# Kernel tuning notes

Measured on AMD Instinct MI355X. Metric: run time of the kernel, lower is better.

Reference implementation:

```python
import jax, jax.numpy as jnp
import numpy as np

B, D, K, E = 256, 256, 1024, 16  # batch, dim_codes, book_size, embedding_dim
DECAY = 0.999
GAIN = 1.0 - DECAY
EPS = 1e-6


def setup_inputs() -> dict:
    key = jax.random.key(0)
    k1, k2 = jax.random.split(key)
    return {
        "cw_q": jax.random.normal(k1, (B, D * E), dtype=jnp.float32),
        "codebook": jax.random.normal(k2, (D, K, E), dtype=jnp.float32),
        "ema_counts": jnp.ones((D, K), dtype=jnp.float32),
    }


def reference(cw_q, codebook, ema_counts):
    batch = cw_q.shape[0]
    x = cw_q.reshape(batch, D, E)  # [B, D, E]

    x2 = jnp.sum(x * x, axis=-1)                       # [B, D]
    c2 = jnp.sum(codebook * codebook, axis=-1)         # [D, K]
    xc = jnp.einsum('bde,dke->bdk', x, codebook)       # [B, D, K]
    dist = x2[:, :, None] + c2[None, :, :] - 2.0 * xc

    idx = jnp.argmin(dist, axis=-1)                    # [B, D] int32

    # gather nearest code vector per (batch, dim_code)
    cw_embed = codebook[jnp.arange(D)[None, :], idx]   # [B, D, E]
    cw_embed = cw_embed.reshape(batch, D * E)

    one_hot_idx = jax.nn.one_hot(idx, K, dtype=cw_q.dtype)  # [B, D, K]

    # EMA update (training path): scatter-sum of assigned vectors per code
    update = jnp.einsum('bdk,bde->dke', one_hot_idx, x)      # [D, K, E]
    new_codebook = codebook * DECAY + GAIN * update / (ema_counts[:, :, None] + EPS)
    new_ema_counts = DECAY * ema_counts + GAIN * jnp.sum(one_hot_idx, axis=0)

    return cw_embed, one_hot_idx, new_codebook, new_ema_counts
```

## Files before the change

kernel.cpp:

```cpp
#include <hip/hip_runtime.h>
#include <float.h>

#define BB 256
#define DD 256
#define KK 1024
#define EE 16
#define DECAY 0.999f
#define GAIN  0.001f
#define EPS   1e-6f

#define OH_OFF   ((size_t)BB * DD * EE)
#define CB_OFF   (OH_OFF + (size_t)BB * DD * KK)
#define EMA_OFF  (CB_OFF + (size_t)DD * KK * EE)

typedef float f32x4 __attribute__((ext_vector_type(4)));

__device__ __forceinline__ float dot16(const float4& a0, const float4& a1,
                                       const float4& a2, const float4& a3,
                                       const float4& b0, const float4& b1,
                                       const float4& b2, const float4& b3) {
  float s = a0.x * b0.x;
  s = fmaf(a0.y, b0.y, s); s = fmaf(a0.z, b0.z, s); s = fmaf(a0.w, b0.w, s);
  s = fmaf(a1.x, b1.x, s); s = fmaf(a1.y, b1.y, s); s = fmaf(a1.z, b1.z, s); s = fmaf(a1.w, b1.w, s);
  s = fmaf(a2.x, b2.x, s); s = fmaf(a2.y, b2.y, s); s = fmaf(a2.z, b2.z, s); s = fmaf(a2.w, b2.w, s);
  s = fmaf(a3.x, b3.x, s); s = fmaf(a3.y, b3.y, s); s = fmaf(a3.z, b3.z, s); s = fmaf(a3.w, b3.w, s);
  return s;
}

__device__ __forceinline__ unsigned long long packkey(float dist, int k) {
  unsigned u = __float_as_uint(dist);
  unsigned m = ((int)u < 0) ? 0xFFFFFFFFu : 0x80000000u;
  return ((unsigned long long)(u ^ m) << 32) | (unsigned long long)(unsigned)k;
}

__device__ __forceinline__ void ntst4(float4* p, float4 v) {
  f32x4 t = { v.x, v.y, v.z, v.w };
  __builtin_nontemporal_store(t, (f32x4*)p);
}

__global__ __launch_bounds__(1024) void vqvae_main(
    const float* __restrict__ cw_q,
    const float* __restrict__ codebook,
    const float* __restrict__ ema,
    float* __restrict__ out)
{
  __shared__ float4 cb4s[KK * EE / 4];
  __shared__ float4 upd4s[KK * EE / 4];
  __shared__ float  c2s[KK];
  __shared__ float  esh[KK];
  __shared__ float  cnts[KK];
  __shared__ unsigned long long amin[BB];
  __shared__ int    ish[BB];

  const int t = threadIdx.x;
  const int d = blockIdx.x;
  const int w = t >> 6;
  const int l = t & 63;
  const float4 z4 = make_float4(0.f, 0.f, 0.f, 0.f);

  cnts[t] = 0.f;
  if (t < BB) amin[t] = ~0ULL;
  esh[t] = ema[(size_t)d * KK + t];
  #pragma unroll
  for (int i = 0; i < 4; ++i) upd4s[i * 1024 + t] = z4;

  const float4* src4 = (const float4*)codebook + (size_t)d * (KK * EE / 4);
  #pragma unroll
  for (int i = 0; i < 4; ++i) {
    int i4 = i * 1024 + t;
    float4 v = src4[i4];
    cb4s[i4] = v;
    float sq = v.x * v.x;
    sq = fmaf(v.y, v.y, sq);
    sq = fmaf(v.z, v.z, sq);
    sq = fmaf(v.w, v.w, sq);
    sq += __shfl_xor(sq, 1);
    sq += __shfl_xor(sq, 2);
    if ((t & 3) == 0) c2s[i4 >> 2] = sq;
  }

  float4 xv[4][4];
  float  x2[4];
  #pragma unroll
  for (int j = 0; j < 4; ++j) {
    const int b = l + 64 * j;
    const float4* xr = (const float4*)cw_q + (size_t)b * (DD * EE / 4) + d * 4;
    xv[j][0] = xr[0]; xv[j][1] = xr[1]; xv[j][2] = xr[2]; xv[j][3] = xr[3];
  }
  #pragma unroll
  for (int j = 0; j < 4; ++j)
    x2[j] = dot16(xv[j][0], xv[j][1], xv[j][2], xv[j][3],
                  xv[j][0], xv[j][1], xv[j][2], xv[j][3]);

  __syncthreads();

  float best[4] = {FLT_MAX, FLT_MAX, FLT_MAX, FLT_MAX};
  int   bi[4]   = {0, 0, 0, 0};
  const int kbase = w << 6;

  #pragma unroll 2
  for (int s = 0; s < 64; ++s) {
    const int k = kbase + s;
    const float4* p = cb4s + (k << 2);
    float4 c0 = p[0], c1 = p[1], c2v = p[2], c3 = p[3];
    const float c2k = c2s[k];
    #pragma unroll
    for (int j = 0; j < 4; ++j) {
      float dj = dot16(c0, c1, c2v, c3, xv[j][0], xv[j][1], xv[j][2], xv[j][3]);
      float dist = fmaf(-2.f, dj, x2[j] + c2k);
      if (dist < best[j]) { best[j] = dist; bi[j] = k; }
    }
  }
  #pragma unroll
  for (int j = 0; j < 4; ++j)
    atomicMin(&amin[l + 64 * j], packkey(best[j], bi[j]));

  __syncthreads();

  const int e = t & 15;
  const int g = t >> 4;
  float xpre[4];
  #pragma unroll
  for (int i = 0; i < 4; ++i)
    xpre[i] = cw_q[(size_t)(g * 4 + i) * (DD * EE) + (size_t)d * EE + e];

  if (t < BB) {
    const int b = t;
    unsigned long long key = amin[b];
    const int bidx = (int)(unsigned)(key & 0xFFFFFFFFull);

    float4* ce = (float4*)out + (size_t)b * (DD * EE / 4) + d * 4;
    const float4* cwp = cb4s + (bidx << 2);
    ntst4(&ce[0], cwp[0]); ntst4(&ce[1], cwp[1]);
    ntst4(&ce[2], cwp[2]); ntst4(&ce[3], cwp[3]);

    ((int*)(out + OH_OFF))[(size_t)b * (DD * KK) + d] = bidx;

    ish[b] = bidx;
    atomicAdd(&cnts[bidx], 1.0f);
  }
  __syncthreads();

  {
    float* upd = (float*)upd4s;
    #pragma unroll
    for (int i = 0; i < 4; ++i) {
      int k = ish[g * 4 + i];
      atomicAdd(&upd[k * EE + e], xpre[i]);
    }
    float* oe = out + EMA_OFF + (size_t)d * KK;
    __builtin_nontemporal_store(DECAY * esh[t] + GAIN * cnts[t], &oe[t]);
  }
  __syncthreads();

  {
    float4* ocb = (float4*)(out + CB_OFF) + (size_t)d * (KK * EE / 4);
    #pragma unroll
    for (int i = 0; i < 4; ++i) {
      int i4 = i * 1024 + t;
      int k  = i4 >> 2;
      float4 c = cb4s[i4];
      float4 u = upd4s[i4];
      float inv = GAIN / (esh[k] + EPS);
      float4 r;
      r.x = DECAY * c.x + u.x * inv;
      r.y = DECAY * c.y + u.y * inv;
      r.z = DECAY * c.z + u.z * inv;
      r.w = DECAY * c.w + u.w * inv;
      ntst4(&ocb[i4], r);
    }
  }
}

__global__ __launch_bounds__(1024) void vqvae_onehot(float* __restrict__ out)
{
  __shared__ int ksh[DD];
  const int b = blockIdx.x;
  const int t = threadIdx.x;
  float* row = out + OH_OFF + (size_t)b * (DD * KK);

  if (t < DD) ksh[t] = ((const int*)row)[t];
  __syncthreads();

  float4* row4 = (float4*)row;
  const int rel = (t & 255) << 2;
  const int tq  = t >> 8;

  #pragma unroll 4
  for (int i = 0; i < 64; ++i) {
    const int hot = ksh[i * 4 + tq];
    float4 v;
    v.x = (rel     == hot) ? 1.0f : 0.0f;
    v.y = (rel + 1 == hot) ? 1.0f : 0.0f;
    v.z = (rel + 2 == hot) ? 1.0f : 0.0f;
    v.w = (rel + 3 == hot) ? 1.0f : 0.0f;
    ntst4(&row4[i * 1024 + t], v);
  }
}

extern "C" void kernel_launch(void* const* d_in, const int* in_sizes, int n_in,
                              void* d_out, int out_size, void* d_ws, size_t ws_size,
                              hipStream_t stream) {
  const float* cw_q     = (const float*)d_in[0];
  const float* codebook = (const float*)d_in[1];
  const float* ema      = (const float*)d_in[2];
  float* out = (float*)d_out;
  (void)in_sizes; (void)n_in; (void)out_size; (void)d_ws; (void)ws_size;

  vqvae_main<<<dim3(DD), dim3(1024), 0, stream>>>(cw_q, codebook, ema, out);
  vqvae_onehot<<<dim3(BB), dim3(1024), 0, stream>>>(out);
}
```

Baseline: 341.2 us.

## Zero-fill one-hot output inside main kernel, overlapped with distance search

The main kernel now zero-fills the one-hot row matching its block index. Those non-temporal zero stores are interleaved with the argmin distance loop, so the large write stream overlaps with compute. The per-code indices are staged in the last 256 floats of each row, which the zero-fill skips. The second kernel shrinks to a 256-thread pass that writes only the tail and scatters a single 1.0 per (b,d), replacing the full dense compare-and-store rewrite. This relies on BB==DD for the row-to-block mapping and adds subtle tail-overlap handling for the last index.

```diff
diff --git a/kernel.cpp b/kernel.cpp
--- a/kernel.cpp
+++ b/kernel.cpp
@@ -12,6 +12,10 @@
 #define OH_OFF   ((size_t)BB * DD * EE)
 #define CB_OFF   (OH_OFF + (size_t)BB * DD * KK)
 #define EMA_OFF  (CB_OFF + (size_t)DD * KK * EE)
+
+#define ROW      (DD * KK)
+#define TAILF    (ROW - 256)
+#define TAIL4    (ROW / 4 - 64)
 
 typedef float f32x4 __attribute__((ext_vector_type(4)));
 
@@ -58,11 +62,16 @@
   const int l = t & 63;
   const float4 z4 = make_float4(0.f, 0.f, 0.f, 0.f);
 
+  float4* zb4 = (float4*)(out + OH_OFF + (size_t)d * ROW);
+
   cnts[t] = 0.f;
   if (t < BB) amin[t] = ~0ULL;
   esh[t] = ema[(size_t)d * KK + t];
   #pragma unroll
   for (int i = 0; i < 4; ++i) upd4s[i * 1024 + t] = z4;
+
+  #pragma unroll
+  for (int j = 0; j < 8; ++j) ntst4(&zb4[j * 1024 + t], z4);
 
   const float4* src4 = (const float4*)codebook + (size_t)d * (KK * EE / 4);
   #pragma unroll
@@ -98,8 +107,8 @@
   int   bi[4]   = {0, 0, 0, 0};
   const int kbase = w << 6;
 
-  #pragma unroll 2
-  for (int s = 0; s < 64; ++s) {
+  #pragma unroll 1
+  for (int s = 0; s < 56; ++s) {
     const int k = kbase + s;
     const float4* p = cb4s + (k << 2);
     float4 c0 = p[0], c1 = p[1], c2v = p[2], c3 = p[3];
@@ -110,7 +119,23 @@
       float dist = fmaf(-2.f, dj, x2[j] + c2k);
       if (dist < best[j]) { best[j] = dist; bi[j] = k; }
     }
-  }
+    const int f = (8 + s) * 1024 + t;
+    if (f < TAIL4) ntst4(&zb4[f], z4);
+  }
+  #pragma unroll 1
+  for (int s = 56; s < 64; ++s) {
+    const int k = kbase + s;
+    const float4* p = cb4s + (k << 2);
+    float4 c0 = p[0], c1 = p[1], c2v = p[2], c3 = p[3];
+    const float c2k = c2s[k];
+    #pragma unroll
+    for (int j = 0; j < 4; ++j) {
+      float dj = dot16(c0, c1, c2v, c3, xv[j][0], xv[j][1], xv[j][2], xv[j][3]);
+      float dist = fmaf(-2.f, dj, x2[j] + c2k);
+      if (dist < best[j]) { best[j] = dist; bi[j] = k; }
+    }
+  }
+
   #pragma unroll
   for (int j = 0; j < 4; ++j)
     atomicMin(&amin[l + 64 * j], packkey(best[j], bi[j]));
@@ -134,7 +159,7 @@
     ntst4(&ce[0], cwp[0]); ntst4(&ce[1], cwp[1]);
     ntst4(&ce[2], cwp[2]); ntst4(&ce[3], cwp[3]);
 
-    ((int*)(out + OH_OFF))[(size_t)b * (DD * KK) + d] = bidx;
+    ((int*)(out + OH_OFF))[(size_t)b * ROW + TAILF + d] = bidx;
 
     ish[b] = bidx;
     atomicAdd(&cnts[bidx], 1.0f);
@@ -172,30 +197,20 @@
   }
 }
 
-__global__ __launch_bounds__(1024) void vqvae_onehot(float* __restrict__ out)
+__global__ __launch_bounds__(256) void vqvae_ones(float* __restrict__ out)
 {
   __shared__ int ksh[DD];
   const int b = blockIdx.x;
   const int t = threadIdx.x;
-  float* row = out + OH_OFF + (size_t)b * (DD * KK);
-
-  if (t < DD) ksh[t] = ((const int*)row)[t];
-  __syncthreads();
-
-  float4* row4 = (float4*)row;
-  const int rel = (t & 255) << 2;
-  const int tq  = t >> 8;
-
-  #pragma unroll 4
-  for (int i = 0; i < 64; ++i) {
-    const int hot = ksh[i * 4 + tq];
-    float4 v;
-    v.x = (rel     == hot) ? 1.0f : 0.0f;
-    v.y = (rel + 1 == hot) ? 1.0f : 0.0f;
-    v.z = (rel + 2 == hot) ? 1.0f : 0.0f;
-    v.w = (rel + 3 == hot) ? 1.0f : 0.0f;
-    ntst4(&row4[i * 1024 + t], v);
-  }
+  float* row = out + OH_OFF + (size_t)b * ROW;
+
+  ksh[t] = ((const int*)row)[TAILF + t];
+  __syncthreads();
+
+  const int k255 = ksh[255];
+  row[TAILF + t] = (768 + t == k255) ? 1.0f : 0.0f;
+  if (t < 255 || k255 < 768)
+    row[(size_t)t * KK + ksh[t]] = 1.0f;
 }
 
 extern "C" void kernel_launch(void* const* d_in, const int* in_sizes, int n_in,
@@ -208,5 +223,5 @@
   (void)in_sizes; (void)n_in; (void)out_size; (void)d_ws; (void)ws_size;
 
   vqvae_main<<<dim3(DD), dim3(1024), 0, stream>>>(cw_q, codebook, ema, out);
-  vqvae_onehot<<<dim3(BB), dim3(1024), 0, stream>>>(out);
-}
+  vqvae_ones<<<dim3(BB), dim3(256), 0, stream>>>(out);
+}
```

Result: no change. 336.7 us (-1.3%).
